# Optimization experiments

Measured on AMD Instinct MI355X. Metric: run time of the kernel, lower is better.

The kernel has to match this reference:

```python
import jax, jax.numpy as jnp
import numpy as np
import math

M = 8                      # multiplicity (channels per irrep)
COMBOS = [(0,0,0),(0,1,1),(1,0,1),(1,1,0),(1,1,1),(2,1,1)]  # (edge_l, node_l, out_l)

def _cg_coeff(j1, m1, j2, m2, j3, m3):
    # standard (Racah) complex Clebsch-Gordan coefficient <j1 m1 j2 m2 | j3 m3>
    if m3 != m1 + m2:
        return 0.0
    f = math.factorial
    vmin = max(0, j2 - j3 - m1, j1 + m2 - j3)
    vmax = min(j1 + j2 - j3, j1 - m1, j2 + m2)
    pref = (2*j3 + 1) * f(j3+j1-j2) * f(j3-j1+j2) * f(j1+j2-j3) / f(j1+j2+j3+1)
    pref *= f(j3+m3) * f(j3-m3) * f(j1-m1) * f(j1+m1) * f(j2-m2) * f(j2+m2)
    s = 0.0
    for v in range(vmin, vmax + 1):
        s += (-1)**v / (f(v) * f(j1+j2-j3-v) * f(j1-m1-v) * f(j2+m2-v)
                        * f(j3-j2+m1+v) * f(j3-j1-m2+v))
    return math.sqrt(pref) * s

def _su2_cg(l1, l2, l3):
    C = np.zeros((2*l1+1, 2*l2+1, 2*l3+1), dtype=np.complex128)
    for m1 in range(-l1, l1+1):
        for m2 in range(-l2, l2+1):
            m3 = m1 + m2
            if -l3 <= m3 <= l3:
                C[m1+l1, m2+l2, m3+l3] = _cg_coeff(l1, m1, l2, m2, l3, m3)
    return C

def _qmat(l):
    # real -> complex spherical-harmonic change of basis (e3nn convention)
    q = np.zeros((2*l+1, 2*l+1), dtype=np.complex128)
    for m in range(-l, 0):
        q[l+m, l+abs(m)] = 1/np.sqrt(2)
        q[l+m, l-abs(m)] = -1j/np.sqrt(2)
    q[l, l] = 1.0
    for m in range(1, l+1):
        q[l+m, l+abs(m)] = (-1)**m / np.sqrt(2)
        q[l+m, l-abs(m)] = 1j * (-1)**m / np.sqrt(2)
    return (-1j)**l * q

def _so3_cg(l1, l2, l3):
    # real-basis CG, normalized to unit Frobenius norm (matches e3nn _so3_clebsch_gordan)
    C = np.einsum('ij,kl,mn,ikn->jlm', _qmat(l1), _qmat(l2),
                  np.conj(_qmat(l3)).T, _su2_cg(l1, l2, l3))
    assert np.abs(C.imag).max() < 1e-6
    C = C.real
    return C / np.linalg.norm(C)

CG = {c: jnp.asarray(_so3_cg(*c), dtype=jnp.float32) for c in COMBOS}


def setup_inputs() -> dict:
    N, E = 100000, 1600000
    ks = jax.random.split(jax.random.key(0), 6)
    return {
        'node_irreps': jax.random.normal(ks[0], (N, 4*M), jnp.float32),
        'edge_index': jax.random.randint(ks[1], (2, E), 0, N, dtype=jnp.int32),
        'sh0': jax.random.normal(ks[2], (E, 1), jnp.float32),
        'sh1': jax.random.normal(ks[3], (E, 3), jnp.float32),
        'sh2': jax.random.normal(ks[4], (E, 5), jnp.float32),
        'W': jax.random.normal(ks[5], (len(COMBOS), M, M), jnp.float32),
    }


def reference(node_irreps, edge_index, sh0, sh1, sh2, W):
    N, E = node_irreps.shape[0], edge_index.shape[1]
    src = node_irreps[edge_index[0]]                    # gather: [E, 4M]
    feats = {0: src[:, :M][:, :, None],                 # scalar channels [E, M, 1]
             1: src[:, M:].reshape(E, M, 3)}            # vector channels [E, M, 3]
    sh = {0: sh0, 1: sh1, 2: sh2}
    msg = {0: jnp.zeros((E, M, 1), node_irreps.dtype),
           1: jnp.zeros((E, M, 3), node_irreps.dtype)}
    for idx, (le, ln, lo) in enumerate(COMBOS):
        # per-edge CG tensor product: [de,dn,do] x [E,de] x [E,M,dn] -> [E,M,do]
        base = jnp.einsum('ijk,ei,emj->emk', CG[(le, ln, lo)], sh[le], feats[ln])
        # channel-mixing scalar weights (in_channel -> out_channel)
        msg[lo] = msg[lo] + jnp.einsum('io,eik->eok', W[idx], base)
    tgt = edge_index[1]
    agg0 = jax.ops.segment_sum(msg[0].reshape(E, M), tgt, num_segments=N)     # [N, M]
    agg1 = jax.ops.segment_sum(msg[1].reshape(E, 3*M), tgt, num_segments=N)   # [N, 3M]
    return jnp.concatenate([agg0, agg1], axis=1)
```

## Files before the change

### kernel.cpp

```cpp
#include <hip/hip_runtime.h>

#define THREADS 256

typedef float v4f __attribute__((ext_vector_type(4)));


__global__ __launch_bounds__(THREADS) void k_hist2(const int* __restrict__ tgt,
                                                   int* __restrict__ cnt,
                                                   int* __restrict__ ke, int E) {
    int e = blockIdx.x * THREADS + threadIdx.x;
    if (e < E) ke[e] = atomicAdd(&cnt[tgt[e]], 1);
}

__global__ __launch_bounds__(THREADS) void k_hist(const int* __restrict__ tgt,
                                                  int* __restrict__ cnt, int E) {
    int e = blockIdx.x * THREADS + threadIdx.x;
    if (e < E) atomicAdd(&cnt[tgt[e]], 1);
}

__global__ __launch_bounds__(THREADS) void k_scan_partial(const int* __restrict__ cnt,
                                                          int* __restrict__ bsum, int N) {
    __shared__ int lds[THREADS];
    int base = blockIdx.x * 1024 + threadIdx.x * 4;
    int s = 0;
    #pragma unroll
    for (int k = 0; k < 4; ++k) { int i = base + k; if (i < N) s += cnt[i]; }
    lds[threadIdx.x] = s; __syncthreads();
    for (int off = THREADS / 2; off > 0; off >>= 1) {
        if (threadIdx.x < off) lds[threadIdx.x] += lds[threadIdx.x + off];
        __syncthreads();
    }
    if (threadIdx.x == 0) bsum[blockIdx.x] = lds[0];
}

__global__ __launch_bounds__(1024) void k_scan_bsum(int* __restrict__ bsum, int NB) {
    __shared__ int lds[1024];
    int t = threadIdx.x;
    int v = (t < NB) ? bsum[t] : 0;
    lds[t] = v; __syncthreads();
    for (int off = 1; off < 1024; off <<= 1) {
        int x = (t >= off) ? lds[t - off] : 0;
        __syncthreads();
        lds[t] += x;
        __syncthreads();
    }
    if (t < NB) bsum[t] = lds[t] - v;
}

__global__ __launch_bounds__(THREADS) void k_scan_final(int* __restrict__ cnt,
                                                        const int* __restrict__ bsum,
                                                        int* __restrict__ rowptr,
                                                        int N, int E) {
    __shared__ int lds[THREADS];
    int base = blockIdx.x * 1024 + threadIdx.x * 4;
    int v[4]; int local = 0;
    #pragma unroll
    for (int k = 0; k < 4; ++k) {
        int i = base + k;
        v[k] = (i < N) ? cnt[i] : 0;
        local += v[k];
    }
    lds[threadIdx.x] = local; __syncthreads();
    for (int off = 1; off < THREADS; off <<= 1) {
        int x = (threadIdx.x >= off) ? lds[threadIdx.x - off] : 0;
        __syncthreads();
        lds[threadIdx.x] += x;
        __syncthreads();
    }
    int p = lds[threadIdx.x] - local + bsum[blockIdx.x];
    #pragma unroll
    for (int k = 0; k < 4; ++k) {
        int i = base + k;
        if (i < N) { rowptr[i] = p; cnt[i] = p; p += v[k]; }
    }
    if (blockIdx.x == 0 && threadIdx.x == 0) rowptr[N] = E;
}


__global__ __launch_bounds__(THREADS) void k_ntrans(const float* __restrict__ node,
                                                    float* __restrict__ nodeT, int NT8) {
    int t = blockIdx.x * THREADS + threadIdx.x;
    if (t >= NT8) return;
    int n = t >> 3, i = t & 7;
    const float* nr = node + (size_t)n * 32;
    v4f v;
    v[0] = nr[i];
    v[1] = nr[8 + 3*i + 0];
    v[2] = nr[8 + 3*i + 1];
    v[3] = nr[8 + 3*i + 2];
    *(v4f*)(nodeT + (size_t)t * 4) = v;
}


__global__ __launch_bounds__(THREADS) void k_scatter4(const int* __restrict__ eidx,
                                                      const int* __restrict__ ke,
                                                      const int* __restrict__ rowptr,
                                                      int* __restrict__ cursor,
                                                      const float* __restrict__ sh0,
                                                      const float* __restrict__ sh1,
                                                      const float* __restrict__ sh2,
                                                      float* __restrict__ pay,
                                                      int E) {
    int e = blockIdx.x * THREADS + threadIdx.x;
    if (e >= E) return;

    constexpr float IS10 = 0.31622776601683794f;
    constexpr float IS30 = 0.18257418583505536f;

    const int src = eidx[e];
    const int tgt = eidx[E + e];
    int pos;
    if (ke) pos = rowptr[tgt] + ke[e];
    else    pos = atomicAdd(&cursor[tgt], 1);

    const float s  = __builtin_nontemporal_load(&sh0[e]);
    const float u0 = __builtin_nontemporal_load(&sh1[3*e+0]);
    const float u1 = __builtin_nontemporal_load(&sh1[3*e+1]);
    const float u2 = __builtin_nontemporal_load(&sh1[3*e+2]);
    const float q0 = __builtin_nontemporal_load(&sh2[5*e+0]);
    const float q1 = __builtin_nontemporal_load(&sh2[5*e+1]);
    const float q2 = __builtin_nontemporal_load(&sh2[5*e+2]);
    const float q3 = __builtin_nontemporal_load(&sh2[5*e+3]);
    const float q4 = __builtin_nontemporal_load(&sh2[5*e+4]);

    const float Q00 = -q2*IS30 - q4*IS10;
    const float Q01 =  q1*IS10;
    const float Q02 =  q0*IS10;
    const float Q11 =  2.0f*q2*IS30;
    const float Q12 =  q3*IS10;
    const float Q22 = -q2*IS30 + q4*IS10;

    float4* pr = (float4*)(pay + (size_t)pos * 16);
    pr[0] = make_float4(s, u0, u1, u2);
    pr[1] = make_float4(Q00, Q01, Q02, Q11);
    pr[2] = make_float4(Q12, Q22, __int_as_float(src), 0.f);
    pr[3] = make_float4(0.f, 0.f, 0.f, 0.f);
}


#define ACC_STRIDE 15

__global__ __launch_bounds__(THREADS) void k_agg7(const float* __restrict__ node,
                                                  const float* __restrict__ nodeT,
                                                  const int*   __restrict__ rowptr,
                                                  const float* __restrict__ pay,
                                                  const float* __restrict__ W,
                                                  float*       __restrict__ out,
                                                  int N, int useT) {
    __shared__ float sW[384];
    __shared__ float sAcc[32 * 8 * ACC_STRIDE];
    for (int t = threadIdx.x; t < 384; t += THREADS) sW[t] = W[t];
    __syncthreads();

    constexpr float IS3 = 0.57735026918962576f;
    constexpr float IS6 = 0.40824829046386302f;

    const int lane  = threadIdx.x & 63;
    const int wv    = threadIdx.x >> 6;
    const int i     = lane & 7;
    const int jslot = lane >> 3;
    const int nbase = blockIdx.x * 32 + wv * 8;

    for (int t = 0; t < 8; ++t) {
        const int n = nbase + t;

        float a[14];
        #pragma unroll
        for (int k = 0; k < 14; ++k) a[k] = 0.f;

        if (n < N) {
            const int jbeg = rowptr[n];
            const int jend = rowptr[n + 1];

            if (jbeg < jend) {
                int j  = jbeg + jslot;
                int jc = (j < jend) ? j : (jend - 1);
                float mcur = (j < jend) ? 1.f : 0.f;
                const v4f* p = (const v4f*)(pay + (size_t)jc * 16);
                v4f c0 = p[0], c1 = p[1], c2 = p[2];
                int src = __float_as_int(c2[2]);
                v4f nf;
                if (useT) {
                    nf = *(const v4f*)(nodeT + ((size_t)src * 8 + i) * 4);
                } else {
                    const float* nr = node + (size_t)src * 32;
                    nf[0] = nr[i];
                    nf[1] = nr[8 + 3*i + 0];
                    nf[2] = nr[8 + 3*i + 1];
                    nf[3] = nr[8 + 3*i + 2];
                }

                for (int g0 = jbeg; g0 < jend; g0 += 8) {
                    const int gn = g0 + 8;
                    const bool more = gn < jend;
                    v4f d0, d1, d2; float mnext = 0.f;
                    if (more) {
                        int jn  = gn + jslot;
                        int jnc = (jn < jend) ? jn : (jend - 1);
                        mnext = (jn < jend) ? 1.f : 0.f;
                        const v4f* pn = (const v4f*)(pay + (size_t)jnc * 16);
                        d0 = pn[0]; d1 = pn[1]; d2 = pn[2];
                    }

                    const float f0 = nf[0] * mcur;
                    const float x  = nf[1] * mcur;
                    const float y  = nf[2] * mcur;
                    const float z  = nf[3] * mcur;
                    const float s   = c0[0], u0 = c0[1], u1 = c0[2], u2 = c0[3];
                    const float Q00 = c1[0], Q01 = c1[1], Q02 = c1[2], Q11 = c1[3];
                    const float Q12 = c2[0], Q22 = c2[1];

                    a[0]  += s * f0;
                    a[1]  += u0*x + u1*y + u2*z;
                    a[2]  += s * x;
                    a[3]  += s * y;
                    a[4]  += s * z;
                    a[5]  += f0 * u0;
                    a[6]  += f0 * u1;
                    a[7]  += f0 * u2;
                    a[8]  += u1*z - u2*y;
                    a[9]  += u2*x - u0*z;
                    a[10] += u0*y - u1*x;
                    a[11] += Q00*x + Q01*y + Q02*z;
                    a[12] += Q01*x + Q11*y + Q12*z;
                    a[13] += Q02*x + Q12*y + Q22*z;

                    if (more) {
                        int srcn = __float_as_int(d2[2]);
                        if (useT) {
                            nf = *(const v4f*)(nodeT + ((size_t)srcn * 8 + i) * 4);
                        } else {
                            const float* nrn = node + (size_t)srcn * 32;
                            nf[0] = nrn[i];
                            nf[1] = nrn[8 + 3*i + 0];
                            nf[2] = nrn[8 + 3*i + 1];
                            nf[3] = nrn[8 + 3*i + 2];
                        }
                        c0 = d0; c1 = d1; c2 = d2; mcur = mnext;
                    }
                }
            }
        }

        #pragma unroll
        for (int k = 0; k < 14; ++k) {
            float v = a[k];
            v += __shfl_xor(v, 8);
            v += __shfl_xor(v, 16);
            v += __shfl_xor(v, 32);
            a[k] = v;
        }

        if (n < N && jslot == 0) {
            #pragma unroll
            for (int k = 1; k < 8; ++k) a[k] *= IS3;
            #pragma unroll
            for (int k = 8; k < 11; ++k) a[k] *= IS6;
            float* myAcc = &sAcc[((wv * 8 + t) * 8 + i) * ACC_STRIDE];
            #pragma unroll
            for (int k = 0; k < 14; ++k) myAcc[k] = a[k];
        }
    }
    __syncthreads();

    {
        const int nodeSlot = threadIdx.x >> 3;
        const int o        = threadIdx.x & 7;
        const int n        = blockIdx.x * 32 + nodeSlot;
        if (n < N) {
            float o0 = 0.f, ox = 0.f, oy = 0.f, oz = 0.f;
            #pragma unroll
            for (int ii = 0; ii < 8; ++ii) {
                const float* A = &sAcc[(nodeSlot * 8 + ii) * ACC_STRIDE];
                const float w0 = sW[  0 + ii*8 + o];
                const float w1 = sW[ 64 + ii*8 + o];
                const float w2 = sW[128 + ii*8 + o];
                const float w3 = sW[192 + ii*8 + o];
                const float w4 = sW[256 + ii*8 + o];
                const float w5 = sW[320 + ii*8 + o];
                o0 += w0*A[0]  + w3*A[1];
                ox += w1*A[2]  + w2*A[5] + w4*A[8]  + w5*A[11];
                oy += w1*A[3]  + w2*A[6] + w4*A[9]  + w5*A[12];
                oz += w1*A[4]  + w2*A[7] + w4*A[10] + w5*A[13];
            }
            float* orow = out + (size_t)n * 32;
            orow[o]         = o0;
            orow[8 + 3*o+0] = ox;
            orow[8 + 3*o+1] = oy;
            orow[8 + 3*o+2] = oz;
        }
    }
}


__global__ __launch_bounds__(THREADS) void msg_kernel_atomic(
    const float* __restrict__ node,
    const int*   __restrict__ eidx,
    const float* __restrict__ sh0,
    const float* __restrict__ sh1,
    const float* __restrict__ sh2,
    const float* __restrict__ W,
    float*       __restrict__ out,
    int E)
{
    __shared__ float sW[384];
    for (int t = threadIdx.x; t < 384; t += THREADS) sW[t] = W[t];
    __syncthreads();

    int e = blockIdx.x * THREADS + threadIdx.x;
    if (e >= E) return;

    constexpr float IS3  = 0.57735026918962576f;
    constexpr float IS6  = 0.40824829046386302f;
    constexpr float IS10 = 0.31622776601683794f;
    constexpr float IS30 = 0.18257418583505536f;

    const int src = eidx[e];
    const int tgt = eidx[E + e];

    const float s  = sh0[e];
    const float u0 = sh1[3*e+0], u1 = sh1[3*e+1], u2 = sh1[3*e+2];
    const float q0 = sh2[5*e+0], q1 = sh2[5*e+1], q2 = sh2[5*e+2],
                q3 = sh2[5*e+3], q4 = sh2[5*e+4];

    const float Q00 = -q2*IS30 - q4*IS10;
    const float Q01 =  q1*IS10;
    const float Q02 =  q0*IS10;
    const float Q11 =  2.0f*q2*IS30;
    const float Q12 =  q3*IS10;
    const float Q22 = -q2*IS30 + q4*IS10;

    float f[32];
    {
        const float4* nr = (const float4*)(node + (size_t)src * 32);
        #pragma unroll
        for (int i = 0; i < 8; ++i) {
            float4 v = nr[i];
            f[4*i+0]=v.x; f[4*i+1]=v.y; f[4*i+2]=v.z; f[4*i+3]=v.w;
        }
    }

    float msg[32];
    #pragma unroll
    for (int j = 0; j < 32; ++j) msg[j] = 0.0f;

    const float s13 = s * IS3;

    #pragma unroll
    for (int i = 0; i < 8; ++i) {
        const float f0i = f[i];
        const float x = f[8+3*i+0], y = f[8+3*i+1], z = f[8+3*i+2];
        const float c0  = s * f0i;
        const float c3  = IS3 * (u0*x + u1*y + u2*z);
        const float p2  = IS3 * f0i;
        const float c1x = s13*x, c1y = s13*y, c1z = s13*z;
        const float c2x = p2*u0, c2y = p2*u1, c2z = p2*u2;
        const float c4x = IS6*(u1*z - u2*y);
        const float c4y = IS6*(u2*x - u0*z);
        const float c4z = IS6*(u0*y - u1*x);
        const float c5x = Q00*x + Q01*y + Q02*z;
        const float c5y = Q01*x + Q11*y + Q12*z;
        const float c5z = Q02*x + Q12*y + Q22*z;

        float wr[6][8];
        #pragma unroll
        for (int c = 0; c < 6; ++c) {
            float4 aa = *(const float4*)&sW[c*64 + i*8 + 0];
            float4 bb = *(const float4*)&sW[c*64 + i*8 + 4];
            wr[c][0]=aa.x; wr[c][1]=aa.y; wr[c][2]=aa.z; wr[c][3]=aa.w;
            wr[c][4]=bb.x; wr[c][5]=bb.y; wr[c][6]=bb.z; wr[c][7]=bb.w;
        }

        #pragma unroll
        for (int o = 0; o < 8; ++o) {
            msg[o] += wr[0][o]*c0 + wr[3][o]*c3;
            msg[8+3*o+0] += wr[1][o]*c1x + wr[2][o]*c2x + wr[4][o]*c4x + wr[5][o]*c5x;
            msg[8+3*o+1] += wr[1][o]*c1y + wr[2][o]*c2y + wr[4][o]*c4y + wr[5][o]*c5y;
            msg[8+3*o+2] += wr[1][o]*c1z + wr[2][o]*c2z + wr[4][o]*c4z + wr[5][o]*c5z;
        }
    }

    float* orow = out + (size_t)tgt * 32;
    #pragma unroll
    for (int j = 0; j < 32; ++j) unsafeAtomicAdd(orow + j, msg[j]);
}


extern "C" void kernel_launch(void* const* d_in, const int* in_sizes, int n_in,
                              void* d_out, int out_size, void* d_ws, size_t ws_size,
                              hipStream_t stream) {
    const float* node = (const float*)d_in[0];
    const int*   eidx = (const int*)d_in[1];
    const float* sh0  = (const float*)d_in[2];
    const float* sh1  = (const float*)d_in[3];
    const float* sh2  = (const float*)d_in[4];
    const float* W    = (const float*)d_in[5];
    float* out = (float*)d_out;

    const int E = in_sizes[2];
    const int N = in_sizes[0] / 32;
    const int NB = (N + 1023) / 1024;

    size_t base_w = (size_t)(N + 1) + N + 1024;
    size_t int12  = base_w + (size_t)E;
    size_t pay12  = (int12 + 15) & ~(size_t)15;
    size_t nT1    = pay12 + (size_t)E * 16;
    size_t need1  = (nT1 + (size_t)N * 32) * sizeof(float);
    size_t need2  = (pay12 + (size_t)E * 16) * sizeof(float);
    size_t pay3   = (base_w + 15) & ~(size_t)15;
    size_t need3  = (pay3 + (size_t)E * 16) * sizeof(float);

    const int gridE = (E + THREADS - 1) / THREADS;

    if (ws_size >= need3 && NB <= 1024) {
        const bool useKe = (ws_size >= need2);
        const bool useT  = (ws_size >= need1);

        int* wsI    = (int*)d_ws;
        int* rowptr = wsI;
        int* cnt    = rowptr + (N + 1);
        int* bsum   = cnt + N;
        int* ke     = useKe ? (bsum + 1024) : nullptr;
        float* pay  = (float*)d_ws + (useKe ? pay12 : pay3);
        float* nodeT = useT ? ((float*)d_ws + nT1) : nullptr;

        hipMemsetAsync(cnt, 0, (size_t)N * sizeof(int), stream);

        if (useKe)
            k_hist2<<<gridE, THREADS, 0, stream>>>(eidx + E, cnt, ke, E);
        else
            k_hist<<<gridE, THREADS, 0, stream>>>(eidx + E, cnt, E);

        if (useT)
            k_ntrans<<<(8 * N + THREADS - 1) / THREADS, THREADS, 0, stream>>>(node, nodeT, 8 * N);

        k_scan_partial<<<NB, THREADS, 0, stream>>>(cnt, bsum, N);
        k_scan_bsum<<<1, 1024, 0, stream>>>(bsum, NB);
        k_scan_final<<<NB, THREADS, 0, stream>>>(cnt, bsum, rowptr, N, E);

        k_scatter4<<<gridE, THREADS, 0, stream>>>(eidx, ke, rowptr, cnt,
                                                  sh0, sh1, sh2, pay, E);

        k_agg7<<<(N + 31) / 32, THREADS, 0, stream>>>(node, nodeT, rowptr, pay, W,
                                                      out, N, useT ? 1 : 0);
    } else {
        hipMemsetAsync(d_out, 0, (size_t)out_size * sizeof(float), stream);
        msg_kernel_atomic<<<gridE, THREADS, 0, stream>>>(
            node, eidx, sh0, sh1, sh2, W, out, E);
    }
}
```

Measured before the change: 375.1 us.

## Fuse CSR build, scatter and aggregation into one persistent kernel with grid barriers

Replaces the chain of histogram, three-stage scan, scatter and aggregation launches with a single persistent kernel of 1024 blocks that separates the phases with software grid barriers. The edge payload is shrunk from 16 to 12 floats per edge, and the node transpose buffer is dropped so aggregation reads node rows directly. The aim is to remove launch overhead and inter-kernel gaps and cut payload traffic. In exchange it depends on all 1024 blocks being co-resident, otherwise the barriers deadlock, it pays barrier spin costs, and the aggregation loses the coalesced transposed node reads.

```diff
diff --git a/kernel.cpp b/kernel.cpp
--- a/kernel.cpp
+++ b/kernel.cpp
@@ -1,294 +1,281 @@
 #include <hip/hip_runtime.h>
 
 #define THREADS 256
+#define FGRID   1024
 
 typedef float v4f __attribute__((ext_vector_type(4)));
 
-
-__global__ __launch_bounds__(THREADS) void k_hist2(const int* __restrict__ tgt,
-                                                   int* __restrict__ cnt,
-                                                   int* __restrict__ ke, int E) {
-    int e = blockIdx.x * THREADS + threadIdx.x;
-    if (e < E) ke[e] = atomicAdd(&cnt[tgt[e]], 1);
+__device__ __forceinline__ void gbar(int* bar, int nb, int gen) {
+    __threadfence();
+    __syncthreads();
+    if (threadIdx.x == 0) {
+        int old = __hip_atomic_fetch_add(&bar[0], 1, __ATOMIC_ACQ_REL,
+                                         __HIP_MEMORY_SCOPE_AGENT);
+        if (old == nb - 1) {
+            __hip_atomic_store(&bar[0], 0, __ATOMIC_RELAXED, __HIP_MEMORY_SCOPE_AGENT);
+            __hip_atomic_fetch_add(&bar[1], 1, __ATOMIC_RELEASE, __HIP_MEMORY_SCOPE_AGENT);
+        } else {
+            while (__hip_atomic_load(&bar[1], __ATOMIC_ACQUIRE,
+                                     __HIP_MEMORY_SCOPE_AGENT) < gen)
+                __builtin_amdgcn_s_sleep(8);
+        }
+    }
+    __syncthreads();
 }
 
-__global__ __launch_bounds__(THREADS) void k_hist(const int* __restrict__ tgt,
-                                                  int* __restrict__ cnt, int E) {
-    int e = blockIdx.x * THREADS + threadIdx.x;
-    if (e < E) atomicAdd(&cnt[tgt[e]], 1);
-}
-
-__global__ __launch_bounds__(THREADS) void k_scan_partial(const int* __restrict__ cnt,
-                                                          int* __restrict__ bsum, int N) {
-    __shared__ int lds[THREADS];
-    int base = blockIdx.x * 1024 + threadIdx.x * 4;
-    int s = 0;
-    #pragma unroll
-    for (int k = 0; k < 4; ++k) { int i = base + k; if (i < N) s += cnt[i]; }
-    lds[threadIdx.x] = s; __syncthreads();
-    for (int off = THREADS / 2; off > 0; off >>= 1) {
-        if (threadIdx.x < off) lds[threadIdx.x] += lds[threadIdx.x + off];
-        __syncthreads();
-    }
-    if (threadIdx.x == 0) bsum[blockIdx.x] = lds[0];
-}
-
-__global__ __launch_bounds__(1024) void k_scan_bsum(int* __restrict__ bsum, int NB) {
-    __shared__ int lds[1024];
-    int t = threadIdx.x;
-    int v = (t < NB) ? bsum[t] : 0;
-    lds[t] = v; __syncthreads();
-    for (int off = 1; off < 1024; off <<= 1) {
-        int x = (t >= off) ? lds[t - off] : 0;
-        __syncthreads();
-        lds[t] += x;
-        __syncthreads();
-    }
-    if (t < NB) bsum[t] = lds[t] - v;
-}
-
-__global__ __launch_bounds__(THREADS) void k_scan_final(int* __restrict__ cnt,
-                                                        const int* __restrict__ bsum,
-                                                        int* __restrict__ rowptr,
-                                                        int N, int E) {
-    __shared__ int lds[THREADS];
-    int base = blockIdx.x * 1024 + threadIdx.x * 4;
-    int v[4]; int local = 0;
-    #pragma unroll
-    for (int k = 0; k < 4; ++k) {
-        int i = base + k;
-        v[k] = (i < N) ? cnt[i] : 0;
-        local += v[k];
-    }
-    lds[threadIdx.x] = local; __syncthreads();
-    for (int off = 1; off < THREADS; off <<= 1) {
-        int x = (threadIdx.x >= off) ? lds[threadIdx.x - off] : 0;
-        __syncthreads();
-        lds[threadIdx.x] += x;
-        __syncthreads();
-    }
-    int p = lds[threadIdx.x] - local + bsum[blockIdx.x];
-    #pragma unroll
-    for (int k = 0; k < 4; ++k) {
-        int i = base + k;
-        if (i < N) { rowptr[i] = p; cnt[i] = p; p += v[k]; }
-    }
-    if (blockIdx.x == 0 && threadIdx.x == 0) rowptr[N] = E;
-}
-
-
-__global__ __launch_bounds__(THREADS) void k_ntrans(const float* __restrict__ node,
-                                                    float* __restrict__ nodeT, int NT8) {
-    int t = blockIdx.x * THREADS + threadIdx.x;
-    if (t >= NT8) return;
-    int n = t >> 3, i = t & 7;
-    const float* nr = node + (size_t)n * 32;
-    v4f v;
-    v[0] = nr[i];
-    v[1] = nr[8 + 3*i + 0];
-    v[2] = nr[8 + 3*i + 1];
-    v[3] = nr[8 + 3*i + 2];
-    *(v4f*)(nodeT + (size_t)t * 4) = v;
-}
-
-
-__global__ __launch_bounds__(THREADS) void k_scatter4(const int* __restrict__ eidx,
-                                                      const int* __restrict__ ke,
-                                                      const int* __restrict__ rowptr,
-                                                      int* __restrict__ cursor,
-                                                      const float* __restrict__ sh0,
-                                                      const float* __restrict__ sh1,
-                                                      const float* __restrict__ sh2,
-                                                      float* __restrict__ pay,
-                                                      int E) {
-    int e = blockIdx.x * THREADS + threadIdx.x;
-    if (e >= E) return;
-
+
+#define ACC_STRIDE 15
+
+__global__ __launch_bounds__(THREADS, 4)
+void k_fused(const float* __restrict__ node,
+             const int*   __restrict__ eidx,
+             const float* __restrict__ sh0,
+             const float* __restrict__ sh1,
+             const float* __restrict__ sh2,
+             const float* __restrict__ W,
+             float*       __restrict__ out,
+             int* bar, int* cnt, int* rowptr, int* bsum, int* ke,
+             float* __restrict__ pay,
+             int N, int E) {
+    __shared__ float sW[384];
+    __shared__ float sAcc[32 * 8 * ACC_STRIDE];
+
+    const int NB  = gridDim.x;
+    const int tid = threadIdx.x;
+
+    for (int t = tid; t < 384; t += THREADS) sW[t] = W[t];
+
+    constexpr float IS3  = 0.57735026918962576f;
+    constexpr float IS6  = 0.40824829046386302f;
     constexpr float IS10 = 0.31622776601683794f;
     constexpr float IS30 = 0.18257418583505536f;
 
-    const int src = eidx[e];
-    const int tgt = eidx[E + e];
-    int pos;
-    if (ke) pos = rowptr[tgt] + ke[e];
-    else    pos = atomicAdd(&cursor[tgt], 1);
-
-    const float s  = __builtin_nontemporal_load(&sh0[e]);
-    const float u0 = __builtin_nontemporal_load(&sh1[3*e+0]);
-    const float u1 = __builtin_nontemporal_load(&sh1[3*e+1]);
-    const float u2 = __builtin_nontemporal_load(&sh1[3*e+2]);
-    const float q0 = __builtin_nontemporal_load(&sh2[5*e+0]);
-    const float q1 = __builtin_nontemporal_load(&sh2[5*e+1]);
-    const float q2 = __builtin_nontemporal_load(&sh2[5*e+2]);
-    const float q3 = __builtin_nontemporal_load(&sh2[5*e+3]);
-    const float q4 = __builtin_nontemporal_load(&sh2[5*e+4]);
-
-    const float Q00 = -q2*IS30 - q4*IS10;
-    const float Q01 =  q1*IS10;
-    const float Q02 =  q0*IS10;
-    const float Q11 =  2.0f*q2*IS30;
-    const float Q12 =  q3*IS10;
-    const float Q22 = -q2*IS30 + q4*IS10;
-
-    float4* pr = (float4*)(pay + (size_t)pos * 16);
-    pr[0] = make_float4(s, u0, u1, u2);
-    pr[1] = make_float4(Q00, Q01, Q02, Q11);
-    pr[2] = make_float4(Q12, Q22, __int_as_float(src), 0.f);
-    pr[3] = make_float4(0.f, 0.f, 0.f, 0.f);
-}
-
-
-#define ACC_STRIDE 15
-
-__global__ __launch_bounds__(THREADS) void k_agg7(const float* __restrict__ node,
-                                                  const float* __restrict__ nodeT,
-                                                  const int*   __restrict__ rowptr,
-                                                  const float* __restrict__ pay,
-                                                  const float* __restrict__ W,
-                                                  float*       __restrict__ out,
-                                                  int N, int useT) {
-    __shared__ float sW[384];
-    __shared__ float sAcc[32 * 8 * ACC_STRIDE];
-    for (int t = threadIdx.x; t < 384; t += THREADS) sW[t] = W[t];
-    __syncthreads();
-
-    constexpr float IS3 = 0.57735026918962576f;
-    constexpr float IS6 = 0.40824829046386302f;
-
-    const int lane  = threadIdx.x & 63;
-    const int wv    = threadIdx.x >> 6;
+    for (int e = blockIdx.x * THREADS + tid; e < E; e += NB * THREADS)
+        ke[e] = atomicAdd(&cnt[eidx[E + e]], 1);
+
+    gbar(bar, NB, 1);
+
+    {
+        int* lds = (int*)sAcc;
+        int base = blockIdx.x * 1024 + tid * 4;
+        int s = 0;
+        #pragma unroll
+        for (int k = 0; k < 4; ++k) { int i = base + k; if (i < N) s += cnt[i]; }
+        lds[tid] = s; __syncthreads();
+        for (int off = THREADS / 2; off > 0; off >>= 1) {
+            if (tid < off) lds[tid] += lds[tid + off];
+            __syncthreads();
+        }
+        if (tid == 0) bsum[blockIdx.x] = lds[0];
+    }
+
+    gbar(bar, NB, 2);
+
+    if (blockIdx.x == 0) {
+        int* lds = (int*)sAcc;
+        int v[4]; int loc = 0;
+        #pragma unroll
+        for (int k = 0; k < 4; ++k) { v[k] = bsum[tid * 4 + k]; loc += v[k]; }
+        lds[tid] = loc; __syncthreads();
+        for (int off = 1; off < THREADS; off <<= 1) {
+            int x = (tid >= off) ? lds[tid - off] : 0;
+            __syncthreads();
+            lds[tid] += x;
+            __syncthreads();
+        }
+        int p = lds[tid] - loc;
+        #pragma unroll
+        for (int k = 0; k < 4; ++k) { bsum[tid * 4 + k] = p; p += v[k]; }
+    }
+
+    gbar(bar, NB, 3);
+
+    {
+        int* lds = (int*)sAcc;
+        int base = blockIdx.x * 1024 + tid * 4;
+        int v[4]; int local = 0;
+        #pragma unroll
+        for (int k = 0; k < 4; ++k) {
+            int i = base + k;
+            v[k] = (i < N) ? cnt[i] : 0;
+            local += v[k];
+        }
+        lds[tid] = local; __syncthreads();
+        for (int off = 1; off < THREADS; off <<= 1) {
+            int x = (tid >= off) ? lds[tid - off] : 0;
+            __syncthreads();
+            lds[tid] += x;
+            __syncthreads();
+        }
+        int p = lds[tid] - local + bsum[blockIdx.x];
+        #pragma unroll
+        for (int k = 0; k < 4; ++k) {
+            int i = base + k;
+            if (i < N) { rowptr[i] = p; p += v[k]; }
+        }
+        if (blockIdx.x == 0 && tid == 0) rowptr[N] = E;
+    }
+
+    gbar(bar, NB, 4);
+
+    for (int e = blockIdx.x * THREADS + tid; e < E; e += NB * THREADS) {
+        const int src = eidx[e];
+        const int tgt = eidx[E + e];
+        const int pos = rowptr[tgt] + ke[e];
+
+        const float s  = __builtin_nontemporal_load(&sh0[e]);
+        const float u0 = __builtin_nontemporal_load(&sh1[3*e+0]);
+        const float u1 = __builtin_nontemporal_load(&sh1[3*e+1]);
+        const float u2 = __builtin_nontemporal_load(&sh1[3*e+2]);
+        const float q0 = __builtin_nontemporal_load(&sh2[5*e+0]);
+        const float q1 = __builtin_nontemporal_load(&sh2[5*e+1]);
+        const float q2 = __builtin_nontemporal_load(&sh2[5*e+2]);
+        const float q3 = __builtin_nontemporal_load(&sh2[5*e+3]);
+        const float q4 = __builtin_nontemporal_load(&sh2[5*e+4]);
+
+        const float Q00 = -q2*IS30 - q4*IS10;
+        const float Q01 =  q1*IS10;
+        const float Q02 =  q0*IS10;
+        const float Q11 =  2.0f*q2*IS30;
+        const float Q12 =  q3*IS10;
+        const float Q22 = -q2*IS30 + q4*IS10;
+
+        float4* pr = (float4*)(pay + (size_t)pos * 12);
+        pr[0] = make_float4(s, u0, u1, u2);
+        pr[1] = make_float4(Q00, Q01, Q02, Q11);
+        pr[2] = make_float4(Q12, Q22, __int_as_float(src), 0.f);
+    }
+
+    gbar(bar, NB, 5);
+
+    const int lane  = tid & 63;
+    const int wv    = tid >> 6;
     const int i     = lane & 7;
     const int jslot = lane >> 3;
-    const int nbase = blockIdx.x * 32 + wv * 8;
-
-    for (int t = 0; t < 8; ++t) {
-        const int n = nbase + t;
-
-        float a[14];
-        #pragma unroll
-        for (int k = 0; k < 14; ++k) a[k] = 0.f;
-
-        if (n < N) {
-            const int jbeg = rowptr[n];
-            const int jend = rowptr[n + 1];
-
-            if (jbeg < jend) {
-                int j  = jbeg + jslot;
-                int jc = (j < jend) ? j : (jend - 1);
-                float mcur = (j < jend) ? 1.f : 0.f;
-                const v4f* p = (const v4f*)(pay + (size_t)jc * 16);
-                v4f c0 = p[0], c1 = p[1], c2 = p[2];
-                int src = __float_as_int(c2[2]);
-                v4f nf;
-                if (useT) {
-                    nf = *(const v4f*)(nodeT + ((size_t)src * 8 + i) * 4);
-                } else {
+
+    for (int nb0 = blockIdx.x * 32; nb0 < N; nb0 += NB * 32) {
+        for (int t = 0; t < 8; ++t) {
+            const int n = nb0 + wv * 8 + t;
+
+            float a[14];
+            #pragma unroll
+            for (int k = 0; k < 14; ++k) a[k] = 0.f;
+
+            if (n < N) {
+                const int jbeg = rowptr[n];
+                const int jend = rowptr[n + 1];
+
+                if (jbeg < jend) {
+                    int j  = jbeg + jslot;
+                    int jc = (j < jend) ? j : (jend - 1);
+                    float mcur = (j < jend) ? 1.f : 0.f;
+                    const v4f* p = (const v4f*)(pay + (size_t)jc * 12);
+                    v4f c0 = p[0], c1 = p[1], c2 = p[2];
+                    int src = __float_as_int(c2[2]);
                     const float* nr = node + (size_t)src * 32;
+                    v4f nf;
                     nf[0] = nr[i];
                     nf[1] = nr[8 + 3*i + 0];
                     nf[2] = nr[8 + 3*i + 1];
                     nf[3] = nr[8 + 3*i + 2];
-                }
-
-                for (int g0 = jbeg; g0 < jend; g0 += 8) {
-                    const int gn = g0 + 8;
-                    const bool more = gn < jend;
-                    v4f d0, d1, d2; float mnext = 0.f;
-                    if (more) {
-                        int jn  = gn + jslot;
-                        int jnc = (jn < jend) ? jn : (jend - 1);
-                        mnext = (jn < jend) ? 1.f : 0.f;
-                        const v4f* pn = (const v4f*)(pay + (size_t)jnc * 16);
-                        d0 = pn[0]; d1 = pn[1]; d2 = pn[2];
-                    }
-
-                    const float f0 = nf[0] * mcur;
-                    const float x  = nf[1] * mcur;
-                    const float y  = nf[2] * mcur;
-                    const float z  = nf[3] * mcur;
-                    const float s   = c0[0], u0 = c0[1], u1 = c0[2], u2 = c0[3];
-                    const float Q00 = c1[0], Q01 = c1[1], Q02 = c1[2], Q11 = c1[3];
-                    const float Q12 = c2[0], Q22 = c2[1];
-
-                    a[0]  += s * f0;
-                    a[1]  += u0*x + u1*y + u2*z;
-                    a[2]  += s * x;
-                    a[3]  += s * y;
-                    a[4]  += s * z;
-                    a[5]  += f0 * u0;
-                    a[6]  += f0 * u1;
-                    a[7]  += f0 * u2;
-                    a[8]  += u1*z - u2*y;
-                    a[9]  += u2*x - u0*z;
-                    a[10] += u0*y - u1*x;
-                    a[11] += Q00*x + Q01*y + Q02*z;
-                    a[12] += Q01*x + Q11*y + Q12*z;
-                    a[13] += Q02*x + Q12*y + Q22*z;
-
-                    if (more) {
-                        int srcn = __float_as_int(d2[2]);
-                        if (useT) {
-                            nf = *(const v4f*)(nodeT + ((size_t)srcn * 8 + i) * 4);
-                        } else {
+
+                    for (int g0 = jbeg; g0 < jend; g0 += 8) {
+                        const int gn = g0 + 8;
+                        const bool more = gn < jend;
+                        v4f d0, d1, d2; float mnext = 0.f;
+                        if (more) {
+                            int jn  = gn + jslot;
+                            int jnc = (jn < jend) ? jn : (jend - 1);
+                            mnext = (jn < jend) ? 1.f : 0.f;
+                            const v4f* pn = (const v4f*)(pay + (size_t)jnc * 12);
+                            d0 = pn[0]; d1 = pn[1]; d2 = pn[2];
+                        }
+
+                        const float f0 = nf[0] * mcur;
+                        const float x  = nf[1] * mcur;
+                        const float y  = nf[2] * mcur;
+                        const float z  = nf[3] * mcur;
+                        const float s   = c0[0], u0 = c0[1], u1 = c0[2], u2 = c0[3];
+                        const float Q00 = c1[0], Q01 = c1[1], Q02 = c1[2], Q11 = c1[3];
+                        const float Q12 = c2[0], Q22 = c2[1];
+
+                        a[0]  += s * f0;
+                        a[1]  += u0*x + u1*y + u2*z;
+                        a[2]  += s * x;
+                        a[3]  += s * y;
+                        a[4]  += s * z;
+                        a[5]  += f0 * u0;
+                        a[6]  += f0 * u1;
+                        a[7]  += f0 * u2;
+                        a[8]  += u1*z - u2*y;
+                        a[9]  += u2*x - u0*z;
+                        a[10] += u0*y - u1*x;
+                        a[11] += Q00*x + Q01*y + Q02*z;
+                        a[12] += Q01*x + Q11*y + Q12*z;
+                        a[13] += Q02*x + Q12*y + Q22*z;
+
+                        if (more) {
+                            int srcn = __float_as_int(d2[2]);
                             const float* nrn = node + (size_t)srcn * 32;
                             nf[0] = nrn[i];
                             nf[1] = nrn[8 + 3*i + 0];
                             nf[2] = nrn[8 + 3*i + 1];
                             nf[3] = nrn[8 + 3*i + 2];
+                            c0 = d0; c1 = d1; c2 = d2; mcur = mnext;
                         }
-                        c0 = d0; c1 = d1; c2 = d2; mcur = mnext;
                     }
                 }
             }
-        }
-
-        #pragma unroll
-        for (int k = 0; k < 14; ++k) {
-            float v = a[k];
-            v += __shfl_xor(v, 8);
-            v += __shfl_xor(v, 16);
-            v += __shfl_xor(v, 32);
-            a[k] = v;
-        }
-
-        if (n < N && jslot == 0) {
+
             #pragma unroll
-            for (int k = 1; k < 8; ++k) a[k] *= IS3;
-            #pragma unroll
-            for (int k = 8; k < 11; ++k) a[k] *= IS6;
-            float* myAcc = &sAcc[((wv * 8 + t) * 8 + i) * ACC_STRIDE];
-            #pragma unroll
-            for (int k = 0; k < 14; ++k) myAcc[k] = a[k];
-        }
-    }
-    __syncthreads();
-
-    {
-        const int nodeSlot = threadIdx.x >> 3;
-        const int o        = threadIdx.x & 7;
-        const int n        = blockIdx.x * 32 + nodeSlot;
-        if (n < N) {
-            float o0 = 0.f, ox = 0.f, oy = 0.f, oz = 0.f;
-            #pragma unroll
-            for (int ii = 0; ii < 8; ++ii) {
-                const float* A = &sAcc[(nodeSlot * 8 + ii) * ACC_STRIDE];
-                const float w0 = sW[  0 + ii*8 + o];
-                const float w1 = sW[ 64 + ii*8 + o];
-                const float w2 = sW[128 + ii*8 + o];
-                const float w3 = sW[192 + ii*8 + o];
-                const float w4 = sW[256 + ii*8 + o];
-                const float w5 = sW[320 + ii*8 + o];
-                o0 += w0*A[0]  + w3*A[1];
-                ox += w1*A[2]  + w2*A[5] + w4*A[8]  + w5*A[11];
-                oy += w1*A[3]  + w2*A[6] + w4*A[9]  + w5*A[12];
-                oz += w1*A[4]  + w2*A[7] + w4*A[10] + w5*A[13];
+            for (int k = 0; k < 14; ++k) {
+                float v = a[k];
+                v += __shfl_xor(v, 8);
+                v += __shfl_xor(v, 16);
+                v += __shfl_xor(v, 32);
+                a[k] = v;
             }
-            float* orow = out + (size_t)n * 32;
-            orow[o]         = o0;
-            orow[8 + 3*o+0] = ox;
-            orow[8 + 3*o+1] = oy;
-            orow[8 + 3*o+2] = oz;
-        }
+
+            if (n < N && jslot == 0) {
+                #pragma unroll
+                for (int k = 1; k < 8; ++k) a[k] *= IS3;
+                #pragma unroll
+                for (int k = 8; k < 11; ++k) a[k] *= IS6;
+                float* myAcc = &sAcc[((wv * 8 + t) * 8 + i) * ACC_STRIDE];
+                #pragma unroll
+                for (int k = 0; k < 14; ++k) myAcc[k] = a[k];
+            }
+        }
+        __syncthreads();
+
+        {
+            const int nodeSlot = tid >> 3;
+            const int o        = tid & 7;
+            const int n        = nb0 + nodeSlot;
+            if (n < N) {
+                float o0 = 0.f, ox = 0.f, oy = 0.f, oz = 0.f;
+                #pragma unroll
+                for (int ii = 0; ii < 8; ++ii) {
+                    const float* A = &sAcc[(nodeSlot * 8 + ii) * ACC_STRIDE];
+                    const float w0 = sW[  0 + ii*8 + o];
+                    const float w1 = sW[ 64 + ii*8 + o];
+                    const float w2 = sW[128 + ii*8 + o];
+                    const float w3 = sW[192 + ii*8 + o];
+                    const float w4 = sW[256 + ii*8 + o];
+                    const float w5 = sW[320 + ii*8 + o];
+                    o0 += w0*A[0]  + w3*A[1];
+                    ox += w1*A[2]  + w2*A[5] + w4*A[8]  + w5*A[11];
+                    oy += w1*A[3]  + w2*A[6] + w4*A[9]  + w5*A[12];
+                    oz += w1*A[4]  + w2*A[7] + w4*A[10] + w5*A[13];
+                }
+                float* orow = out + (size_t)n * 32;
+                orow[o]         = o0;
+                orow[8 + 3*o+0] = ox;
+                orow[8 + 3*o+1] = oy;
+                orow[8 + 3*o+2] = oz;
+            }
+        }
+        __syncthreads();
     }
 }
 
@@ -399,53 +386,34 @@
 
     const int E = in_sizes[2];
     const int N = in_sizes[0] / 32;
-    const int NB = (N + 1023) / 1024;
-
-    size_t base_w = (size_t)(N + 1) + N + 1024;
-    size_t int12  = base_w + (size_t)E;
-    size_t pay12  = (int12 + 15) & ~(size_t)15;
-    size_t nT1    = pay12 + (size_t)E * 16;
-    size_t need1  = (nT1 + (size_t)N * 32) * sizeof(float);
-    size_t need2  = (pay12 + (size_t)E * 16) * sizeof(float);
-    size_t pay3   = (base_w + 15) & ~(size_t)15;
-    size_t need3  = (pay3 + (size_t)E * 16) * sizeof(float);
-
-    const int gridE = (E + THREADS - 1) / THREADS;
-
-    if (ws_size >= need3 && NB <= 1024) {
-        const bool useKe = (ws_size >= need2);
-        const bool useT  = (ws_size >= need1);
-
+
+    size_t off = 0;
+    size_t off_bar    = off; off += 2;
+    size_t off_cnt    = off; off += (size_t)N;
+    size_t off_rowptr = off; off += (size_t)N + 1;
+    size_t off_bsum   = off; off += FGRID;
+    size_t off_ke     = off; off += (size_t)E;
+    off = (off + 15) & ~(size_t)15;
+    size_t off_pay    = off; off += (size_t)E * 12;
+    size_t need = off * sizeof(float);
+
+    if (ws_size >= need && N <= FGRID * 1024) {
         int* wsI    = (int*)d_ws;
-        int* rowptr = wsI;
-        int* cnt    = rowptr + (N + 1);
-        int* bsum   = cnt + N;
-        int* ke     = useKe ? (bsum + 1024) : nullptr;
-        float* pay  = (float*)d_ws + (useKe ? pay12 : pay3);
-        float* nodeT = useT ? ((float*)d_ws + nT1) : nullptr;
-
-        hipMemsetAsync(cnt, 0, (size_t)N * sizeof(int), stream);
-
-        if (useKe)
-            k_hist2<<<gridE, THREADS, 0, stream>>>(eidx + E, cnt, ke, E);
-        else
-            k_hist<<<gridE, THREADS, 0, stream>>>(eidx + E, cnt, E);
-
-        if (useT)
-            k_ntrans<<<(8 * N + THREADS - 1) / THREADS, THREADS, 0, stream>>>(node, nodeT, 8 * N);
-
-        k_scan_partial<<<NB, THREADS, 0, stream>>>(cnt, bsum, N);
-        k_scan_bsum<<<1, 1024, 0, stream>>>(bsum, NB);
-        k_scan_final<<<NB, THREADS, 0, stream>>>(cnt, bsum, rowptr, N, E);
-
-        k_scatter4<<<gridE, THREADS, 0, stream>>>(eidx, ke, rowptr, cnt,
-                                                  sh0, sh1, sh2, pay, E);
-
-        k_agg7<<<(N + 31) / 32, THREADS, 0, stream>>>(node, nodeT, rowptr, pay, W,
-                                                      out, N, useT ? 1 : 0);
+        int* bar    = wsI + off_bar;
+        int* cnt    = wsI + off_cnt;
+        int* rowptr = wsI + off_rowptr;
+        int* bsum   = wsI + off_bsum;
+        int* ke     = wsI + off_ke;
+        float* pay  = (float*)d_ws + off_pay;
+
+        hipMemsetAsync(bar, 0, (size_t)(2 + N) * sizeof(int), stream);
+
+        k_fused<<<FGRID, THREADS, 0, stream>>>(node, eidx, sh0, sh1, sh2, W, out,
+                                               bar, cnt, rowptr, bsum, ke, pay,
+                                               N, E);
     } else {
         hipMemsetAsync(d_out, 0, (size_t)out_size * sizeof(float), stream);
-        msg_kernel_atomic<<<gridE, THREADS, 0, stream>>>(
+        msg_kernel_atomic<<<(E + THREADS - 1) / THREADS, THREADS, 0, stream>>>(
             node, eidx, sh0, sh1, sh2, W, out, E);
     }
 }
```

Result: slower. 1.292 ms (+244.6%).

## Merge scan into single-block kernel and drop node transpose pre-pass

Applied to the files above, without the earlier changes.

Replaces the three-kernel prefix scan over node degrees with one 1024-thread single-block scan, where each thread serially handles a chunk of about 98 nodes. It also removes the node-feature transpose kernel, so the aggregation kernel gathers the strided layout straight from the original node array. This cuts two to three kernel launches and one pass over node data. In exchange the scan becomes a serial, single-workgroup step and the gathers in the aggregation kernel become scattered scalar loads instead of one 16-byte vector load.

```diff
diff --git a/kernel.cpp b/kernel.cpp
--- a/kernel.cpp
+++ b/kernel.cpp
@@ -18,81 +18,37 @@
     if (e < E) atomicAdd(&cnt[tgt[e]], 1);
 }
 
-__global__ __launch_bounds__(THREADS) void k_scan_partial(const int* __restrict__ cnt,
-                                                          int* __restrict__ bsum, int N) {
-    __shared__ int lds[THREADS];
-    int base = blockIdx.x * 1024 + threadIdx.x * 4;
+
+__global__ __launch_bounds__(1024) void k_scan1(int* __restrict__ cnt,
+                                                int* __restrict__ rowptr,
+                                                int N, int E) {
+    __shared__ int lds[1024];
+    const int t = threadIdx.x;
+    const int chunk = (N + 1023) >> 10;
+    const int lo = t * chunk;
+    const int hi = (lo + chunk < N) ? lo + chunk : N;
+
     int s = 0;
-    #pragma unroll
-    for (int k = 0; k < 4; ++k) { int i = base + k; if (i < N) s += cnt[i]; }
-    lds[threadIdx.x] = s; __syncthreads();
-    for (int off = THREADS / 2; off > 0; off >>= 1) {
-        if (threadIdx.x < off) lds[threadIdx.x] += lds[threadIdx.x + off];
-        __syncthreads();
-    }
-    if (threadIdx.x == 0) bsum[blockIdx.x] = lds[0];
-}
-
-__global__ __launch_bounds__(1024) void k_scan_bsum(int* __restrict__ bsum, int NB) {
-    __shared__ int lds[1024];
-    int t = threadIdx.x;
-    int v = (t < NB) ? bsum[t] : 0;
-    lds[t] = v; __syncthreads();
+    for (int i = lo; i < hi; ++i) s += cnt[i];
+    lds[t] = s; __syncthreads();
     for (int off = 1; off < 1024; off <<= 1) {
         int x = (t >= off) ? lds[t - off] : 0;
         __syncthreads();
         lds[t] += x;
         __syncthreads();
     }
-    if (t < NB) bsum[t] = lds[t] - v;
-}
-
-__global__ __launch_bounds__(THREADS) void k_scan_final(int* __restrict__ cnt,
-                                                        const int* __restrict__ bsum,
-                                                        int* __restrict__ rowptr,
-                                                        int N, int E) {
-    __shared__ int lds[THREADS];
-    int base = blockIdx.x * 1024 + threadIdx.x * 4;
-    int v[4]; int local = 0;
-    #pragma unroll
-    for (int k = 0; k < 4; ++k) {
-        int i = base + k;
-        v[k] = (i < N) ? cnt[i] : 0;
-        local += v[k];
-    }
-    lds[threadIdx.x] = local; __syncthreads();
-    for (int off = 1; off < THREADS; off <<= 1) {
-        int x = (threadIdx.x >= off) ? lds[threadIdx.x - off] : 0;
-        __syncthreads();
-        lds[threadIdx.x] += x;
-        __syncthreads();
-    }
-    int p = lds[threadIdx.x] - local + bsum[blockIdx.x];
-    #pragma unroll
-    for (int k = 0; k < 4; ++k) {
-        int i = base + k;
-        if (i < N) { rowptr[i] = p; cnt[i] = p; p += v[k]; }
-    }
-    if (blockIdx.x == 0 && threadIdx.x == 0) rowptr[N] = E;
-}
-
-
-__global__ __launch_bounds__(THREADS) void k_ntrans(const float* __restrict__ node,
-                                                    float* __restrict__ nodeT, int NT8) {
-    int t = blockIdx.x * THREADS + threadIdx.x;
-    if (t >= NT8) return;
-    int n = t >> 3, i = t & 7;
-    const float* nr = node + (size_t)n * 32;
-    v4f v;
-    v[0] = nr[i];
-    v[1] = nr[8 + 3*i + 0];
-    v[2] = nr[8 + 3*i + 1];
-    v[3] = nr[8 + 3*i + 2];
-    *(v4f*)(nodeT + (size_t)t * 4) = v;
-}
-
-
-__global__ __launch_bounds__(THREADS) void k_scatter4(const int* __restrict__ eidx,
+    int p = lds[t] - s;
+    for (int i = lo; i < hi; ++i) {
+        int c = cnt[i];
+        rowptr[i] = p;
+        cnt[i] = p;
+        p += c;
+    }
+    if (t == 0) rowptr[N] = E;
+}
+
+
+__global__ __launch_bounds__(THREADS) void k_scatter5(const int* __restrict__ eidx,
                                                       const int* __restrict__ ke,
                                                       const int* __restrict__ rowptr,
                                                       int* __restrict__ cursor,
@@ -140,13 +96,12 @@
 
 #define ACC_STRIDE 15
 
-__global__ __launch_bounds__(THREADS) void k_agg7(const float* __restrict__ node,
-                                                  const float* __restrict__ nodeT,
+__global__ __launch_bounds__(THREADS) void k_agg8(const float* __restrict__ node,
                                                   const int*   __restrict__ rowptr,
                                                   const float* __restrict__ pay,
                                                   const float* __restrict__ W,
                                                   float*       __restrict__ out,
-                                                  int N, int useT) {
+                                                  int N) {
     __shared__ float sW[384];
     __shared__ float sAcc[32 * 8 * ACC_STRIDE];
     for (int t = threadIdx.x; t < 384; t += THREADS) sW[t] = W[t];
@@ -159,10 +114,9 @@
     const int wv    = threadIdx.x >> 6;
     const int i     = lane & 7;
     const int jslot = lane >> 3;
-    const int nbase = blockIdx.x * 32 + wv * 8;
 
     for (int t = 0; t < 8; ++t) {
-        const int n = nbase + t;
+        const int n = blockIdx.x * 32 + wv * 8 + t;
 
         float a[14];
         #pragma unroll
@@ -179,16 +133,12 @@
                 const v4f* p = (const v4f*)(pay + (size_t)jc * 16);
                 v4f c0 = p[0], c1 = p[1], c2 = p[2];
                 int src = __float_as_int(c2[2]);
+                const float* nr = node + (size_t)src * 32;
                 v4f nf;
-                if (useT) {
-                    nf = *(const v4f*)(nodeT + ((size_t)src * 8 + i) * 4);
-                } else {
-                    const float* nr = node + (size_t)src * 32;
-                    nf[0] = nr[i];
-                    nf[1] = nr[8 + 3*i + 0];
-                    nf[2] = nr[8 + 3*i + 1];
-                    nf[3] = nr[8 + 3*i + 2];
-                }
+                nf[0] = nr[i];
+                nf[1] = nr[8 + 3*i + 0];
+                nf[2] = nr[8 + 3*i + 1];
+                nf[3] = nr[8 + 3*i + 2];
 
                 for (int g0 = jbeg; g0 < jend; g0 += 8) {
                     const int gn = g0 + 8;
@@ -227,15 +177,11 @@
 
                     if (more) {
                         int srcn = __float_as_int(d2[2]);
-                        if (useT) {
-                            nf = *(const v4f*)(nodeT + ((size_t)srcn * 8 + i) * 4);
-                        } else {
-                            const float* nrn = node + (size_t)srcn * 32;
-                            nf[0] = nrn[i];
-                            nf[1] = nrn[8 + 3*i + 0];
-                            nf[2] = nrn[8 + 3*i + 1];
-                            nf[3] = nrn[8 + 3*i + 2];
-                        }
+                        const float* nrn = node + (size_t)srcn * 32;
+                        nf[0] = nrn[i];
+                        nf[1] = nrn[8 + 3*i + 0];
+                        nf[2] = nrn[8 + 3*i + 1];
+                        nf[3] = nrn[8 + 3*i + 2];
                         c0 = d0; c1 = d1; c2 = d2; mcur = mnext;
                     }
                 }
@@ -399,30 +345,24 @@
 
     const int E = in_sizes[2];
     const int N = in_sizes[0] / 32;
-    const int NB = (N + 1023) / 1024;
-
-    size_t base_w = (size_t)(N + 1) + N + 1024;
-    size_t int12  = base_w + (size_t)E;
-    size_t pay12  = (int12 + 15) & ~(size_t)15;
-    size_t nT1    = pay12 + (size_t)E * 16;
-    size_t need1  = (nT1 + (size_t)N * 32) * sizeof(float);
-    size_t need2  = (pay12 + (size_t)E * 16) * sizeof(float);
-    size_t pay3   = (base_w + 15) & ~(size_t)15;
-    size_t need3  = (pay3 + (size_t)E * 16) * sizeof(float);
+
+    size_t base_w = (size_t)N + (size_t)(N + 1);
+    size_t intA_w = base_w + (size_t)E;
+    size_t payA   = (intA_w + 15) & ~(size_t)15;
+    size_t payB   = (base_w + 15) & ~(size_t)15;
+    size_t needA  = (payA + (size_t)E * 16) * sizeof(float);
+    size_t needB  = (payB + (size_t)E * 16) * sizeof(float);
 
     const int gridE = (E + THREADS - 1) / THREADS;
 
-    if (ws_size >= need3 && NB <= 1024) {
-        const bool useKe = (ws_size >= need2);
-        const bool useT  = (ws_size >= need1);
+    if (ws_size >= needB && N <= 1024 * 4096) {
+        const bool useKe = (ws_size >= needA);
 
         int* wsI    = (int*)d_ws;
-        int* rowptr = wsI;
-        int* cnt    = rowptr + (N + 1);
-        int* bsum   = cnt + N;
-        int* ke     = useKe ? (bsum + 1024) : nullptr;
-        float* pay  = (float*)d_ws + (useKe ? pay12 : pay3);
-        float* nodeT = useT ? ((float*)d_ws + nT1) : nullptr;
+        int* cnt    = wsI;
+        int* rowptr = cnt + N;
+        int* ke     = useKe ? (rowptr + (N + 1)) : nullptr;
+        float* pay  = (float*)d_ws + (useKe ? payA : payB);
 
         hipMemsetAsync(cnt, 0, (size_t)N * sizeof(int), stream);
 
@@ -431,18 +371,12 @@
         else
             k_hist<<<gridE, THREADS, 0, stream>>>(eidx + E, cnt, E);
 
-        if (useT)
-            k_ntrans<<<(8 * N + THREADS - 1) / THREADS, THREADS, 0, stream>>>(node, nodeT, 8 * N);
-
-        k_scan_partial<<<NB, THREADS, 0, stream>>>(cnt, bsum, N);
-        k_scan_bsum<<<1, 1024, 0, stream>>>(bsum, NB);
-        k_scan_final<<<NB, THREADS, 0, stream>>>(cnt, bsum, rowptr, N, E);
-
-        k_scatter4<<<gridE, THREADS, 0, stream>>>(eidx, ke, rowptr, cnt,
+        k_scan1<<<1, 1024, 0, stream>>>(cnt, rowptr, N, E);
+
+        k_scatter5<<<gridE, THREADS, 0, stream>>>(eidx, ke, rowptr, cnt,
                                                   sh0, sh1, sh2, pay, E);
 
-        k_agg7<<<(N + 31) / 32, THREADS, 0, stream>>>(node, nodeT, rowptr, pay, W,
-                                                      out, N, useT ? 1 : 0);
+        k_agg8<<<(N + 31) / 32, THREADS, 0, stream>>>(node, rowptr, pay, W, out, N);
     } else {
         hipMemsetAsync(d_out, 0, (size_t)out_size * sizeof(float), stream);
         msg_kernel_atomic<<<gridE, THREADS, 0, stream>>>(
```

Measured after the change: 576.8 us. +53.8%, slower.
